# Kernel tuning notes

Measured on AMD Instinct MI355X. Metric: run time of the kernel, lower is better.

Reference implementation:

```python
import jax, jax.numpy as jnp
import numpy as np

NEG_SLOPE = 0.2  # PyG GATConv default leaky_relu slope
EPS = 1e-16     # PyG softmax denominator epsilon


def gat_conv(x, src, dst, W, att_src, att_dst, bias, concat, num_nodes):
    """PyG-style GATConv (eval mode, dropout disabled).
    x: [N, F_in]; W: [F_in, H*C]; att_src/att_dst: [H, C]; bias: [H*C] or [C].
    Messages flow src -> dst; softmax is per destination node."""
    H, C = att_src.shape
    h = (x @ W).reshape(num_nodes, H, C)                      # [N,H,C]
    a_src = jnp.sum(h * att_src[None], axis=-1)               # [N,H]
    a_dst = jnp.sum(h * att_dst[None], axis=-1)               # [N,H]
    e = jax.nn.leaky_relu(a_src[src] + a_dst[dst], NEG_SLOPE) # [E,H]
    # numerically-stable segment softmax over edges grouped by dst
    m = jax.ops.segment_max(e, dst, num_segments=num_nodes)   # [N,H]
    ex = jnp.exp(e - m[dst])                                  # [E,H]
    s = jax.ops.segment_sum(ex, dst, num_segments=num_nodes)  # [N,H]
    alpha = ex / (s[dst] + EPS)                               # [E,H]
    msg = h[src] * alpha[..., None]                           # [E,H,C]
    out = jax.ops.segment_sum(msg, dst, num_segments=num_nodes)  # [N,H,C]
    if concat:
        out = out.reshape(num_nodes, H * C)
    else:
        out = out.mean(axis=1)                                # [N,C]
    return out + bias, alpha


def setup_inputs() -> dict:
    key = jax.random.key(0)
    ks = jax.random.split(key, 20)
    N, E = 50000, 500000
    F_node = 128       # num_node_features
    SED = 128          # sentence_embedding_dim
    HID = 64           # hidden_channels
    H = 2              # num_heads

    def g(k, shape, scale=0.05):
        return jax.random.normal(k, shape, dtype=jnp.float32) * scale

    return {
        "x": jax.random.normal(ks[0], (N, SED), dtype=jnp.float32),
        "edge_index": jax.random.randint(ks[1], (2, E), 0, N, dtype=jnp.int64),
        "cls_emb": jax.random.normal(ks[2], (768,), dtype=jnp.float32),
        # fc0: Linear(768, SED)
        "fc0_w": g(ks[3], (SED, 768)), "fc0_b": g(ks[4], (SED,)),
        # conv1: GATConv(2*SED -> HID, heads=H, concat=True)
        "W1": g(ks[5], (2 * SED, H * HID)),
        "att_src1": g(ks[6], (H, HID)), "att_dst1": g(ks[7], (H, HID)),
        "bias1": g(ks[8], (H * HID,)),
        # conv2: GATConv(H*HID -> F_node, heads=H, concat=False)
        "W2": g(ks[9], (H * HID, H * F_node)),
        "att_src2": g(ks[10], (H, F_node)), "att_dst2": g(ks[11], (H, F_node)),
        "bias2": g(ks[12], (F_node,)),
        # edge MLP head
        "fc2_w": g(ks[13], (F_node, 2 * F_node)), "fc2_b": g(ks[14], (F_node,)),
        "fc3_w": g(ks[15], (1, F_node)), "fc3_b": g(ks[16], (1,)),
    }


def reference(x, edge_index, cls_emb, fc0_w, fc0_b,
              W1, att_src1, att_dst1, bias1,
              W2, att_src2, att_dst2, bias2,
              fc2_w, fc2_b, fc3_w, fc3_b):
    N = x.shape[0]
    src, dst = edge_index[0], edge_index[1]
    # sentence embedding projection + broadcast-concat to every node
    sent = fc0_w @ cls_emb + fc0_b                                # [SED]
    h = jnp.concatenate([x, jnp.broadcast_to(sent, (N, sent.shape[0]))], axis=1)
    h, _ = gat_conv(h, src, dst, W1, att_src1, att_dst1, bias1, True, N)
    h = jax.nn.elu(h)
    h, _ = gat_conv(h, src, dst, W2, att_src2, att_dst2, bias2, False, N)
    # edge head: gather endpoints, concat, MLP, sigmoid
    edge_input = jnp.concatenate([h[src], h[dst]], axis=1)        # [E, 2*F]
    z = jax.nn.relu(edge_input @ fc2_w.T + fc2_b)                 # [E, F]
    logits = z @ fc3_w.T + fc3_b                                  # [E, 1]
    return jax.nn.sigmoid(logits)
```

## Files before the change

### kernel.cpp

```cpp
#include <hip/hip_runtime.h>
#include <hip/hip_bf16.h>
#include <math.h>


typedef short short8 __attribute__((ext_vector_type(8)));
typedef float floatx4 __attribute__((ext_vector_type(4)));

__device__ __forceinline__ float wave_allreduce_sum(float v) {
    #pragma unroll
    for (int off = 1; off < 64; off <<= 1) v += __shfl_xor(v, off, 64);
    return v;
}
__device__ __forceinline__ float bf16lo(unsigned u) {
    unsigned x = u << 16; return __builtin_bit_cast(float, x);
}
__device__ __forceinline__ float bf16hi(unsigned u) {
    unsigned x = u & 0xFFFF0000u; return __builtin_bit_cast(float, x);
}
__device__ __forceinline__ unsigned short bfbits(float f) {
    return __builtin_bit_cast(unsigned short, __float2bfloat16(f));
}
__device__ __forceinline__ unsigned packbf(float a, float b) {
    return ((unsigned)bfbits(b) << 16) | (unsigned)bfbits(a);
}
__device__ __forceinline__ float lrelu(float v) { return v > 0.f ? v : 0.2f * v; }

__global__ void prep_kernel(const float* __restrict__ cls, const float* __restrict__ fc0_w,
                            const float* __restrict__ fc0_b, const float* __restrict__ W1,
                            const float* __restrict__ W2, const float* __restrict__ fc2_w,
                            float* __restrict__ c1,
                            __hip_bfloat16* __restrict__ w1frag,
                            __hip_bfloat16* __restrict__ w2frag,
                            __hip_bfloat16* __restrict__ fc2frag) {
    int tid = threadIdx.x;
    if (blockIdx.x == 0) {
        __shared__ float s_sent[128];
        if (tid < 128) {
            float acc = fc0_b[tid];
            const float* row = fc0_w + (size_t)tid * 768;
            for (int k = 0; k < 768; ++k) acc += row[k] * cls[k];
            s_sent[tid] = acc;
        }
        __syncthreads();
        if (tid < 128) {
            float acc = 0.f;
            for (int k = 0; k < 128; ++k) acc += s_sent[k] * W1[(128 + k) * 128 + tid];
            c1[tid] = acc;
        }
    }
    int gstride = gridDim.x * blockDim.x;
    int g = blockIdx.x * blockDim.x + tid;
    for (int i = g; i < 16384; i += gstride) {
        int j = i & 7, l = (i >> 3) & 63, nt = (i >> 9) & 7, kt = (i >> 12) & 3;
        int k = kt * 32 + (l >> 4) * 8 + j;
        int n = nt * 16 + (l & 15);
        w1frag[i] = __float2bfloat16(W1[k * 128 + n]);
    }
    for (int i = g; i < 32768; i += gstride) {
        int j = i & 7, l = (i >> 3) & 63, nt = (i >> 9) & 15, kt = (i >> 13) & 3;
        int k = kt * 32 + (l >> 4) * 8 + j;
        int n = nt * 16 + (l & 15);
        w2frag[i] = __float2bfloat16(W2[k * 256 + n]);
    }
    for (int i = g; i < 32768; i += gstride) {
        int j = i & 7, l = (i >> 3) & 63, nt = (i >> 9) & 15, kt = (i >> 13) & 3;
        int k = kt * 32 + (l >> 4) * 8 + j;
        int n = nt * 16 + (l & 15);
        float v = (n < 128) ? fc2_w[n * 256 + k] : fc2_w[(n - 128) * 256 + 128 + k];
        fc2frag[i] = __float2bfloat16(v);
    }
}

__global__ void count_kernel(const int* __restrict__ dst, int* __restrict__ counts, int E) {
    int e = blockIdx.x * blockDim.x + threadIdx.x;
    if (e < E) atomicAdd(&counts[dst[e]], 1);
}

__global__ void __launch_bounds__(256) bsum_kernel(const int* __restrict__ counts,
                                                   int* __restrict__ bsum, int N) {
    int base = blockIdx.x * 1024;
    int tid = threadIdx.x;
    int v = 0;
    #pragma unroll
    for (int k = 0; k < 4; ++k) {
        int idx = base + k * 256 + tid;
        if (idx < N) v += counts[idx];
    }
    #pragma unroll
    for (int off = 1; off < 64; off <<= 1) v += __shfl_xor(v, off, 64);
    __shared__ int ws[4];
    if ((tid & 63) == 0) ws[tid >> 6] = v;
    __syncthreads();
    if (tid == 0) bsum[blockIdx.x] = ws[0] + ws[1] + ws[2] + ws[3];
}

__global__ void top_scan_kernel(const int* __restrict__ bsum, int* __restrict__ boff, int nb) {
    int lane = threadIdx.x;
    int v = (lane < nb) ? bsum[lane] : 0;
    int x = v;
    #pragma unroll
    for (int off = 1; off < 64; off <<= 1) {
        int t = __shfl_up(x, off, 64);
        if (lane >= off) x += t;
    }
    if (lane < nb) boff[lane] = x - v;
}

__global__ void __launch_bounds__(1024) local_scan_kernel(const int* __restrict__ counts,
                                                          const int* __restrict__ boff,
                                                          int* __restrict__ row, int* __restrict__ woff,
                                                          int N, int E) {
    int tid = threadIdx.x, lane = tid & 63, wv = tid >> 6;
    int base = blockIdx.x * 1024;
    __shared__ int wsum[16];
    int v = (base + tid < N) ? counts[base + tid] : 0;
    int x = v;
    #pragma unroll
    for (int off = 1; off < 64; off <<= 1) {
        int t = __shfl_up(x, off, 64);
        if (lane >= off) x += t;
    }
    if (lane == 63) wsum[wv] = x;
    __syncthreads();
    if (wv == 0 && lane < 16) {
        int y = wsum[lane];
        #pragma unroll
        for (int off = 1; off < 16; off <<= 1) {
            int t = __shfl_up(y, off, 64);
            if (lane >= off) y += t;
        }
        wsum[lane] = y;
    }
    __syncthreads();
    int excl = boff[blockIdx.x] + (wv ? wsum[wv - 1] : 0) + x - v;
    if (base + tid < N) { row[base + tid] = excl; woff[base + tid] = excl; }
    if (blockIdx.x == 0 && tid == 0) row[N] = E;
}

__global__ void scatter_logit1_kernel(const int* __restrict__ src, const int* __restrict__ dst,
                                      int* __restrict__ woff,
                                      const float* __restrict__ a_s1, const float* __restrict__ a_d1,
                                      int* __restrict__ srcs, float2* __restrict__ ex1,
                                      int* __restrict__ epos, int E) {
    int e = blockIdx.x * blockDim.x + threadIdx.x;
    if (e >= E) return;
    int s = src[e], d = dst[e];
    int pos = atomicAdd(&woff[d], 1);
    epos[e] = pos;
    srcs[pos] = s;
    float2 as = ((const float2*)a_s1)[s];
    float2 ad = ((const float2*)a_d1)[d];
    float2 ex;
    ex.x = __expf(lrelu(as.x + ad.x));
    ex.y = __expf(lrelu(as.y + ad.y));
    ex1[pos] = ex;
}

__global__ void logit2_kernel(const int* __restrict__ src, const int* __restrict__ dst,
                              const int* __restrict__ epos,
                              const float* __restrict__ a_s2, const float* __restrict__ a_d2,
                              float2* __restrict__ ex2, int E) {
    int e = blockIdx.x * blockDim.x + threadIdx.x;
    if (e >= E) return;
    int s = src[e], d = dst[e];
    float2 as = ((const float2*)a_s2)[s];
    float2 ad = ((const float2*)a_d2)[d];
    float2 ex;
    ex.x = __expf(lrelu(as.x + ad.x));
    ex.y = __expf(lrelu(as.y + ad.y));
    ex2[epos[e]] = ex;
}

__global__ void __launch_bounds__(256) gemm1_mfma_kernel(
        const float* __restrict__ x, const __hip_bfloat16* __restrict__ wfrag,
        const float* __restrict__ c1, const float* __restrict__ att_s, const float* __restrict__ att_d,
        __hip_bfloat16* __restrict__ h1bf, float* __restrict__ a_src, float* __restrict__ a_dst, int N) {
    int lane = threadIdx.x & 63, wv = threadIdx.x >> 6;
    int lo = lane & 15, quad = lane >> 4;
    int rowbase = (blockIdx.x * 4 + wv) * 16;
    if (rowbase >= N) return;
    int arow = rowbase + lo; if (arow >= N) arow = N - 1;
    const float* ap = x + (size_t)arow * 128 + quad * 8;
    floatx4 acc[8];
    #pragma unroll
    for (int nt = 0; nt < 8; ++nt) acc[nt] = (floatx4){0.f, 0.f, 0.f, 0.f};
    const short8* bf = (const short8*)wfrag;
    #pragma unroll
    for (int kt = 0; kt < 4; ++kt) {
        float4 fa = *(const float4*)(ap + kt * 32);
        float4 fb = *(const float4*)(ap + kt * 32 + 4);
        short8 a;
        a[0] = (short)bfbits(fa.x); a[1] = (short)bfbits(fa.y);
        a[2] = (short)bfbits(fa.z); a[3] = (short)bfbits(fa.w);
        a[4] = (short)bfbits(fb.x); a[5] = (short)bfbits(fb.y);
        a[6] = (short)bfbits(fb.z); a[7] = (short)bfbits(fb.w);
        #pragma unroll
        for (int nt = 0; nt < 8; ++nt)
            acc[nt] = __builtin_amdgcn_mfma_f32_16x16x32_bf16(a, bf[(kt * 8 + nt) * 64 + lane], acc[nt], 0, 0, 0);
    }
    float ps0[4] = {0,0,0,0}, ps1[4] = {0,0,0,0}, pd0[4] = {0,0,0,0}, pd1[4] = {0,0,0,0};
    #pragma unroll
    for (int nt = 0; nt < 8; ++nt) {
        int ch = nt * 16 + lo;
        float cv = c1[ch], as_v = att_s[ch], ad_v = att_d[ch];
        #pragma unroll
        for (int r = 0; r < 4; ++r) {
            int row = rowbase + quad * 4 + r;
            float val = acc[nt][r] + cv;
            if (row < N) ((unsigned short*)h1bf)[(size_t)row * 128 + ch] = bfbits(val);
            if (nt < 4) { ps0[r] += val * as_v; pd0[r] += val * ad_v; }
            else        { ps1[r] += val * as_v; pd1[r] += val * ad_v; }
        }
    }
    #pragma unroll
    for (int r = 0; r < 4; ++r) {
        int row = rowbase + quad * 4 + r;
        float v0 = ps0[r], v1 = ps1[r], v2 = pd0[r], v3 = pd1[r];
        #pragma unroll
        for (int off = 1; off < 16; off <<= 1) {
            v0 += __shfl_xor(v0, off, 64); v1 += __shfl_xor(v1, off, 64);
            v2 += __shfl_xor(v2, off, 64); v3 += __shfl_xor(v3, off, 64);
        }
        if (lo == 0 && row < N) {
            a_src[row * 2 + 0] = v0; a_src[row * 2 + 1] = v1;
            a_dst[row * 2 + 0] = v2; a_dst[row * 2 + 1] = v3;
        }
    }
}

__global__ void __launch_bounds__(256) agg1_csr_kernel(
        const int* __restrict__ row, const int* __restrict__ srcs, const float2* __restrict__ ex1,
        const unsigned* __restrict__ h1u, const float* __restrict__ bias1,
        unsigned* __restrict__ hmid_u, int N) {
    int d = blockIdx.x * 4 + (threadIdx.x >> 6);
    if (d >= N) return;
    int lane = threadIdx.x & 63;
    int beg = row[d], end = row[d + 1];
    int g = lane >> 4, q = lane & 15;
    float den0 = 0.f, den1 = 0.f;
    float facc[8];
    #pragma unroll
    for (int m = 0; m < 8; ++m) facc[m] = 0.f;
    for (int b = beg; b < end; b += 64) {
        int i = b + lane;
        int s = 0; float e0 = 0.f, e1 = 0.f;
        if (i < end) {
            s = srcs[i];
            float2 ex = ex1[i];
            e0 = ex.x; e1 = ex.y;
            den0 += e0; den1 += e1;
        }
        int cnt = min(64, end - b);
        int rounds = (cnt + 3) >> 2;
        for (int j = 0; j < rounds; ++j) {
            int sl = 4 * j + g;
            float w0 = __shfl(e0, sl, 64);
            float w1 = __shfl(e1, sl, 64);
            int   sj = __shfl(s,  sl, 64);
            float wgt = (q < 8) ? w0 : w1;
            uint4 u = ((const uint4*)(h1u + (size_t)sj * 64))[q];
            facc[0] += bf16lo(u.x) * wgt; facc[1] += bf16hi(u.x) * wgt;
            facc[2] += bf16lo(u.y) * wgt; facc[3] += bf16hi(u.y) * wgt;
            facc[4] += bf16lo(u.z) * wgt; facc[5] += bf16hi(u.z) * wgt;
            facc[6] += bf16lo(u.w) * wgt; facc[7] += bf16hi(u.w) * wgt;
        }
    }
    den0 = wave_allreduce_sum(den0);
    den1 = wave_allreduce_sum(den1);
    #pragma unroll
    for (int m = 0; m < 8; ++m) {
        facc[m] += __shfl_xor(facc[m], 16, 64);
        facc[m] += __shfl_xor(facc[m], 32, 64);
    }
    if (lane < 16) {
        float inv = (lane < 8) ? 1.f / (den0 + 1e-16f) : 1.f / (den1 + 1e-16f);
        int c0 = 8 * lane;
        float v[8];
        #pragma unroll
        for (int m = 0; m < 8; ++m) {
            float vv = facc[m] * inv + bias1[c0 + m];
            v[m] = vv > 0.f ? vv : expm1f(vv);
        }
        uint4 o;
        o.x = packbf(v[0], v[1]); o.y = packbf(v[2], v[3]);
        o.z = packbf(v[4], v[5]); o.w = packbf(v[6], v[7]);
        ((uint4*)(hmid_u + (size_t)d * 64))[lane] = o;
    }
}

__global__ void __launch_bounds__(256) gemm2_mfma_kernel(
        const __hip_bfloat16* __restrict__ hmid, const __hip_bfloat16* __restrict__ wfrag,
        const float* __restrict__ att_s, const float* __restrict__ att_d,
        __hip_bfloat16* __restrict__ h2pre, float* __restrict__ a_src, float* __restrict__ a_dst, int N) {
    int lane = threadIdx.x & 63, wv = threadIdx.x >> 6;
    int lo = lane & 15, quad = lane >> 4;
    int rowbase = (blockIdx.x * 4 + wv) * 16;
    if (rowbase >= N) return;
    int arow = rowbase + lo; if (arow >= N) arow = N - 1;
    const __hip_bfloat16* ap = hmid + (size_t)arow * 128 + quad * 8;
    floatx4 acc[16];
    #pragma unroll
    for (int nt = 0; nt < 16; ++nt) acc[nt] = (floatx4){0.f, 0.f, 0.f, 0.f};
    const short8* bf = (const short8*)wfrag;
    #pragma unroll
    for (int kt = 0; kt < 4; ++kt) {
        short8 a = *(const short8*)(ap + kt * 32);
        #pragma unroll
        for (int nt = 0; nt < 16; ++nt)
            acc[nt] = __builtin_amdgcn_mfma_f32_16x16x32_bf16(a, bf[(kt * 16 + nt) * 64 + lane], acc[nt], 0, 0, 0);
    }
    float ps0[4] = {0,0,0,0}, ps1[4] = {0,0,0,0}, pd0[4] = {0,0,0,0}, pd1[4] = {0,0,0,0};
    #pragma unroll
    for (int nt = 0; nt < 16; ++nt) {
        int ch = nt * 16 + lo;
        float as_v = att_s[ch], ad_v = att_d[ch];
        #pragma unroll
        for (int r = 0; r < 4; ++r) {
            int row = rowbase + quad * 4 + r;
            float val = acc[nt][r];
            if (row < N) ((unsigned short*)h2pre)[(size_t)row * 256 + ch] = bfbits(val);
            if (nt < 8) { ps0[r] += val * as_v; pd0[r] += val * ad_v; }
            else        { ps1[r] += val * as_v; pd1[r] += val * ad_v; }
        }
    }
    #pragma unroll
    for (int r = 0; r < 4; ++r) {
        int row = rowbase + quad * 4 + r;
        float v0 = ps0[r], v1 = ps1[r], v2 = pd0[r], v3 = pd1[r];
        #pragma unroll
        for (int off = 1; off < 16; off <<= 1) {
            v0 += __shfl_xor(v0, off, 64); v1 += __shfl_xor(v1, off, 64);
            v2 += __shfl_xor(v2, off, 64); v3 += __shfl_xor(v3, off, 64);
        }
        if (lo == 0 && row < N) {
            a_src[row * 2 + 0] = v0; a_src[row * 2 + 1] = v1;
            a_dst[row * 2 + 0] = v2; a_dst[row * 2 + 1] = v3;
        }
    }
}

__global__ void __launch_bounds__(256) agg2_csr_kernel(
        const int* __restrict__ row, const int* __restrict__ srcs, const float2* __restrict__ ex2,
        const unsigned* __restrict__ h2u, const float* __restrict__ bias2,
        unsigned* __restrict__ h2bf_u, int N) {
    int d = blockIdx.x * 4 + (threadIdx.x >> 6);
    if (d >= N) return;
    int lane = threadIdx.x & 63;
    int beg = row[d], end = row[d + 1];
    int g = lane >> 5, q = lane & 31;
    float den0 = 0.f, den1 = 0.f;
    float facc[8];
    #pragma unroll
    for (int m = 0; m < 8; ++m) facc[m] = 0.f;
    for (int b = beg; b < end; b += 64) {
        int i = b + lane;
        int s = 0; float e0 = 0.f, e1 = 0.f;
        if (i < end) {
            s = srcs[i];
            float2 ex = ex2[i];
            e0 = ex.x; e1 = ex.y;
            den0 += e0; den1 += e1;
        }
        int cnt = min(64, end - b);
        int rounds = (cnt + 1) >> 1;
        for (int j = 0; j < rounds; ++j) {
            int sl = 2 * j + g;
            float w0 = __shfl(e0, sl, 64);
            float w1 = __shfl(e1, sl, 64);
            int   sj = __shfl(s,  sl, 64);
            float wgt = (q < 16) ? w0 : w1;
            uint4 u = ((const uint4*)(h2u + (size_t)sj * 128))[q];
            facc[0] += bf16lo(u.x) * wgt; facc[1] += bf16hi(u.x) * wgt;
            facc[2] += bf16lo(u.y) * wgt; facc[3] += bf16hi(u.y) * wgt;
            facc[4] += bf16lo(u.z) * wgt; facc[5] += bf16hi(u.z) * wgt;
            facc[6] += bf16lo(u.w) * wgt; facc[7] += bf16hi(u.w) * wgt;
        }
    }
    den0 = wave_allreduce_sum(den0);
    den1 = wave_allreduce_sum(den1);
    float inv = (q < 16) ? 0.5f / (den0 + 1e-16f) : 0.5f / (den1 + 1e-16f);
    #pragma unroll
    for (int m = 0; m < 8; ++m) {
        facc[m] += __shfl_xor(facc[m], 32, 64);
        facc[m] *= inv;
        facc[m] += __shfl_xor(facc[m], 16, 64);
    }
    if (lane < 16) {
        int c0 = 8 * lane;
        uint4 o;
        o.x = packbf(facc[0] + bias2[c0 + 0], facc[1] + bias2[c0 + 1]);
        o.y = packbf(facc[2] + bias2[c0 + 2], facc[3] + bias2[c0 + 3]);
        o.z = packbf(facc[4] + bias2[c0 + 4], facc[5] + bias2[c0 + 5]);
        o.w = packbf(facc[6] + bias2[c0 + 6], facc[7] + bias2[c0 + 7]);
        ((uint4*)(h2bf_u + (size_t)d * 64))[lane] = o;
    }
}

__global__ void __launch_bounds__(256) zsd_mfma_kernel(
        const __hip_bfloat16* __restrict__ h2bf, const __hip_bfloat16* __restrict__ wfrag,
        const float* __restrict__ fc2_b, __hip_bfloat16* __restrict__ zsd, int N) {
    int lane = threadIdx.x & 63, wv = threadIdx.x >> 6;
    int lo = lane & 15, quad = lane >> 4;
    int rowbase = (blockIdx.x * 4 + wv) * 16;
    if (rowbase >= N) return;
    int arow = rowbase + lo; if (arow >= N) arow = N - 1;
    const __hip_bfloat16* ap = h2bf + (size_t)arow * 128 + quad * 8;
    floatx4 acc[16];
    #pragma unroll
    for (int nt = 0; nt < 16; ++nt) acc[nt] = (floatx4){0.f, 0.f, 0.f, 0.f};
    const short8* bf = (const short8*)wfrag;
    #pragma unroll
    for (int kt = 0; kt < 4; ++kt) {
        short8 a = *(const short8*)(ap + kt * 32);
        #pragma unroll
        for (int nt = 0; nt < 16; ++nt)
            acc[nt] = __builtin_amdgcn_mfma_f32_16x16x32_bf16(a, bf[(kt * 16 + nt) * 64 + lane], acc[nt], 0, 0, 0);
    }
    #pragma unroll
    for (int nt = 0; nt < 16; ++nt) {
        int ch = nt * 16 + lo;
        float bv = (nt >= 8) ? fc2_b[ch - 128] : 0.f;
        #pragma unroll
        for (int r = 0; r < 4; ++r) {
            int row = rowbase + quad * 4 + r;
            if (row < N) ((unsigned short*)zsd)[(size_t)row * 256 + ch] = bfbits(acc[nt][r] + bv);
        }
    }
}

__global__ void __launch_bounds__(256) edge_zsd_kernel(
        const int* __restrict__ src, const int* __restrict__ dst,
        const unsigned* __restrict__ zsd_u, const float* __restrict__ fc3_w,
        const float* __restrict__ fc3_b, float* __restrict__ out, int E) {
    int lane = threadIdx.x & 63, wv = threadIdx.x >> 6;
    int g = lane >> 5, r = (lane >> 4) & 1, q = lane & 15;
    int base = (blockIdx.x * 4 + wv) * 16;
    if (base >= E) return;
    float f3[8];
    #pragma unroll
    for (int m = 0; m < 8; ++m) f3[m] = fc3_w[8 * q + m];
    float b3 = fc3_b[0];
    #pragma unroll
    for (int j = 0; j < 8; ++j) {
        int e = base + 2 * j + g;
        int ec = e < E ? e : E - 1;
        int node = r ? dst[ec] : src[ec];
        uint4 mine = ((const uint4*)(zsd_u + (size_t)node * 128 + (r << 6)))[q];
        uint4 oth;
        oth.x = (unsigned)__shfl_xor((int)mine.x, 16, 64);
        oth.y = (unsigned)__shfl_xor((int)mine.y, 16, 64);
        oth.z = (unsigned)__shfl_xor((int)mine.z, 16, 64);
        oth.w = (unsigned)__shfl_xor((int)mine.w, 16, 64);
        float p = 0.f;
        p += fmaxf(bf16lo(mine.x) + bf16lo(oth.x), 0.f) * f3[0];
        p += fmaxf(bf16hi(mine.x) + bf16hi(oth.x), 0.f) * f3[1];
        p += fmaxf(bf16lo(mine.y) + bf16lo(oth.y), 0.f) * f3[2];
        p += fmaxf(bf16hi(mine.y) + bf16hi(oth.y), 0.f) * f3[3];
        p += fmaxf(bf16lo(mine.z) + bf16lo(oth.z), 0.f) * f3[4];
        p += fmaxf(bf16hi(mine.z) + bf16hi(oth.z), 0.f) * f3[5];
        p += fmaxf(bf16lo(mine.w) + bf16lo(oth.w), 0.f) * f3[6];
        p += fmaxf(bf16hi(mine.w) + bf16hi(oth.w), 0.f) * f3[7];
        #pragma unroll
        for (int off = 1; off < 32; off <<= 1) p += __shfl_xor(p, off, 64);
        if ((lane & 31) == 0 && e < E)
            out[e] = 1.f / (1.f + expf(-(0.5f * p + b3)));
    }
}

extern "C" void kernel_launch(void* const* d_in, const int* in_sizes, int n_in,
                              void* d_out, int out_size, void* d_ws, size_t ws_size,
                              hipStream_t stream) {
    const float* x      = (const float*)d_in[0];
    const int*   ei     = (const int*)d_in[1];
    const float* cls    = (const float*)d_in[2];
    const float* fc0_w  = (const float*)d_in[3];
    const float* fc0_b  = (const float*)d_in[4];
    const float* W1     = (const float*)d_in[5];
    const float* att_s1 = (const float*)d_in[6];
    const float* att_d1 = (const float*)d_in[7];
    const float* bias1  = (const float*)d_in[8];
    const float* W2     = (const float*)d_in[9];
    const float* att_s2 = (const float*)d_in[10];
    const float* att_d2 = (const float*)d_in[11];
    const float* bias2  = (const float*)d_in[12];
    const float* fc2_w  = (const float*)d_in[13];
    const float* fc2_b  = (const float*)d_in[14];
    const float* fc3_w  = (const float*)d_in[15];
    const float* fc3_b  = (const float*)d_in[16];
    float* out = (float*)d_out;

    int N = in_sizes[0] / 128;
    int E = in_sizes[1] / 2;
    const int* src = ei;
    const int* dst = ei + E;
    int nb = (N + 1023) / 1024;

    float* w = (float*)d_ws;
    size_t off = 0;
    auto alloc = [&](size_t n) { float* p = w + off; off += (n + 63) & ~(size_t)63; return p; };
    float* c1      = alloc(128);
    float* w1fragf = alloc(16384 / 2);
    float* w2fragf = alloc(32768 / 2);
    float* fc2fragf= alloc(32768 / 2);
    float* a_s1    = alloc((size_t)N * 2);
    float* a_d1    = alloc((size_t)N * 2);
    float* a_s2    = alloc((size_t)N * 2);
    float* a_d2    = alloc((size_t)N * 2);
    float* h1bff   = alloc((size_t)N * 64);
    float* hmidf   = alloc((size_t)N * 64);
    float* h2pref  = alloc((size_t)N * 128);
    float* h2bff   = alloc((size_t)N * 64);
    float* zsdf    = alloc((size_t)N * 128);
    float* ex1f    = alloc((size_t)E * 2);
    float* ex2f    = alloc((size_t)E * 2);
    int* counts = (int*)alloc(N);
    int* rowp   = (int*)alloc(N + 1);
    int* woff   = (int*)alloc(N);
    int* srcs   = (int*)alloc(E);
    int* epos   = (int*)alloc(E);
    int* bsum   = (int*)alloc(64);
    int* boff   = (int*)alloc(64);
    __hip_bfloat16* w1frag = (__hip_bfloat16*)w1fragf;
    __hip_bfloat16* w2frag = (__hip_bfloat16*)w2fragf;
    __hip_bfloat16* fc2frag= (__hip_bfloat16*)fc2fragf;
    __hip_bfloat16* h1bf   = (__hip_bfloat16*)h1bff;
    __hip_bfloat16* hmid   = (__hip_bfloat16*)hmidf;
    __hip_bfloat16* h2pre  = (__hip_bfloat16*)h2pref;
    __hip_bfloat16* h2bf   = (__hip_bfloat16*)h2bff;
    __hip_bfloat16* zsd    = (__hip_bfloat16*)zsdf;

    hipMemsetAsync(counts, 0, sizeof(int) * (size_t)N, stream);

    prep_kernel<<<64, 256, 0, stream>>>(cls, fc0_w, fc0_b, W1, W2, fc2_w, c1, w1frag, w2frag, fc2frag);
    count_kernel<<<(E + 255) / 256, 256, 0, stream>>>(dst, counts, E);
    bsum_kernel<<<nb, 256, 0, stream>>>(counts, bsum, N);
    top_scan_kernel<<<1, 64, 0, stream>>>(bsum, boff, nb);
    local_scan_kernel<<<nb, 1024, 0, stream>>>(counts, boff, rowp, woff, N, E);
    gemm1_mfma_kernel<<<(N + 63) / 64, 256, 0, stream>>>(x, w1frag, c1, att_s1, att_d1, h1bf, a_s1, a_d1, N);
    scatter_logit1_kernel<<<(E + 255) / 256, 256, 0, stream>>>(src, dst, woff, a_s1, a_d1, srcs, (float2*)ex1f, epos, E);
    agg1_csr_kernel<<<(N + 3) / 4, 256, 0, stream>>>(rowp, srcs, (const float2*)ex1f, (const unsigned*)h1bf, bias1, (unsigned*)hmid, N);
    gemm2_mfma_kernel<<<(N + 63) / 64, 256, 0, stream>>>(hmid, w2frag, att_s2, att_d2, h2pre, a_s2, a_d2, N);
    logit2_kernel<<<(E + 255) / 256, 256, 0, stream>>>(src, dst, epos, a_s2, a_d2, (float2*)ex2f, E);
    agg2_csr_kernel<<<(N + 3) / 4, 256, 0, stream>>>(rowp, srcs, (const float2*)ex2f, (const unsigned*)h2pre, bias2, (unsigned*)h2bf, N);
    zsd_mfma_kernel<<<(N + 63) / 64, 256, 0, stream>>>(h2bf, fc2frag, fc2_b, zsd, N);
    edge_zsd_kernel<<<(E + 63) / 64, 256, 0, stream>>>(src, dst, (const unsigned*)zsd, fc3_w, fc3_b, out, E);
}
```

Baseline: 375.5 us.

## Fuse edge logits into CSR aggregation, single-block scan, prefetch gathers, packed math

Drops the separate per-edge logit kernels and their ex/epos buffers, and computes the exp-logits inside the aggregation kernels from a_src/a_dst. The three-kernel scan becomes a single 1024-thread block that loops over all nodes. Scatter now only writes srcs. The aggregation inner loops software-prefetch the next neighbour row and accumulate with packed float2 math, and the edge head splits its fc3 work across the two half-waves. The single-block scan serialises about 50 iterations, which risks a longer latency for that step than the old multi-block scan.

```diff
diff --git a/kernel.cpp b/kernel.cpp
--- a/kernel.cpp
+++ b/kernel.cpp
@@ -5,6 +5,8 @@
 
 typedef short short8 __attribute__((ext_vector_type(8)));
 typedef float floatx4 __attribute__((ext_vector_type(4)));
+typedef float v2f __attribute__((ext_vector_type(2)));
+typedef unsigned uint2v __attribute__((ext_vector_type(2)));
 
 __device__ __forceinline__ float wave_allreduce_sum(float v) {
     #pragma unroll
@@ -16,6 +18,10 @@
 }
 __device__ __forceinline__ float bf16hi(unsigned u) {
     unsigned x = u & 0xFFFF0000u; return __builtin_bit_cast(float, x);
+}
+__device__ __forceinline__ v2f bfpair(unsigned v) {
+    uint2v t; t.x = v << 16; t.y = v & 0xFFFF0000u;
+    return __builtin_bit_cast(v2f, t);
 }
 __device__ __forceinline__ unsigned short bfbits(float f) {
     return __builtin_bit_cast(unsigned short, __float2bfloat16(f));
@@ -76,99 +82,51 @@
     if (e < E) atomicAdd(&counts[dst[e]], 1);
 }
 
-__global__ void __launch_bounds__(256) bsum_kernel(const int* __restrict__ counts,
-                                                   int* __restrict__ bsum, int N) {
-    int base = blockIdx.x * 1024;
-    int tid = threadIdx.x;
-    int v = 0;
-    #pragma unroll
-    for (int k = 0; k < 4; ++k) {
-        int idx = base + k * 256 + tid;
-        if (idx < N) v += counts[idx];
-    }
-    #pragma unroll
-    for (int off = 1; off < 64; off <<= 1) v += __shfl_xor(v, off, 64);
-    __shared__ int ws[4];
-    if ((tid & 63) == 0) ws[tid >> 6] = v;
+__global__ void __launch_bounds__(1024) scan_kernel(const int* __restrict__ counts,
+                                                    int* __restrict__ row, int* __restrict__ woff,
+                                                    int N, int E) {
+    int tid = threadIdx.x, lane = tid & 63, wv = tid >> 6;
+    __shared__ int wsum[16];
+    __shared__ int carry;
+    if (tid == 0) carry = 0;
     __syncthreads();
-    if (tid == 0) bsum[blockIdx.x] = ws[0] + ws[1] + ws[2] + ws[3];
-}
-
-__global__ void top_scan_kernel(const int* __restrict__ bsum, int* __restrict__ boff, int nb) {
-    int lane = threadIdx.x;
-    int v = (lane < nb) ? bsum[lane] : 0;
-    int x = v;
-    #pragma unroll
-    for (int off = 1; off < 64; off <<= 1) {
-        int t = __shfl_up(x, off, 64);
-        if (lane >= off) x += t;
-    }
-    if (lane < nb) boff[lane] = x - v;
-}
-
-__global__ void __launch_bounds__(1024) local_scan_kernel(const int* __restrict__ counts,
-                                                          const int* __restrict__ boff,
-                                                          int* __restrict__ row, int* __restrict__ woff,
-                                                          int N, int E) {
-    int tid = threadIdx.x, lane = tid & 63, wv = tid >> 6;
-    int base = blockIdx.x * 1024;
-    __shared__ int wsum[16];
-    int v = (base + tid < N) ? counts[base + tid] : 0;
-    int x = v;
-    #pragma unroll
-    for (int off = 1; off < 64; off <<= 1) {
-        int t = __shfl_up(x, off, 64);
-        if (lane >= off) x += t;
-    }
-    if (lane == 63) wsum[wv] = x;
-    __syncthreads();
-    if (wv == 0 && lane < 16) {
-        int y = wsum[lane];
-        #pragma unroll
-        for (int off = 1; off < 16; off <<= 1) {
-            int t = __shfl_up(y, off, 64);
-            if (lane >= off) y += t;
-        }
-        wsum[lane] = y;
-    }
-    __syncthreads();
-    int excl = boff[blockIdx.x] + (wv ? wsum[wv - 1] : 0) + x - v;
-    if (base + tid < N) { row[base + tid] = excl; woff[base + tid] = excl; }
-    if (blockIdx.x == 0 && tid == 0) row[N] = E;
-}
-
-__global__ void scatter_logit1_kernel(const int* __restrict__ src, const int* __restrict__ dst,
-                                      int* __restrict__ woff,
-                                      const float* __restrict__ a_s1, const float* __restrict__ a_d1,
-                                      int* __restrict__ srcs, float2* __restrict__ ex1,
-                                      int* __restrict__ epos, int E) {
+    for (int base = 0; base < N; base += 1024) {
+        int v = (base + tid < N) ? counts[base + tid] : 0;
+        int x = v;
+        #pragma unroll
+        for (int off = 1; off < 64; off <<= 1) {
+            int t = __shfl_up(x, off, 64);
+            if (lane >= off) x += t;
+        }
+        if (lane == 63) wsum[wv] = x;
+        __syncthreads();
+        if (wv == 0 && lane < 16) {
+            int y = wsum[lane];
+            #pragma unroll
+            for (int off = 1; off < 16; off <<= 1) {
+                int t = __shfl_up(y, off, 64);
+                if (lane >= off) y += t;
+            }
+            wsum[lane] = y;
+        }
+        __syncthreads();
+        int wexcl = (wv == 0) ? 0 : wsum[wv - 1];
+        int excl = carry + wexcl + x - v;
+        if (base + tid < N) { row[base + tid] = excl; woff[base + tid] = excl; }
+        __syncthreads();
+        if (tid == 0) carry += wsum[15];
+        __syncthreads();
+    }
+    if (tid == 0) row[N] = E;
+}
+
+__global__ void scatter_kernel(const int* __restrict__ src, const int* __restrict__ dst,
+                               int* __restrict__ woff, int* __restrict__ srcs, int E) {
     int e = blockIdx.x * blockDim.x + threadIdx.x;
-    if (e >= E) return;
-    int s = src[e], d = dst[e];
-    int pos = atomicAdd(&woff[d], 1);
-    epos[e] = pos;
-    srcs[pos] = s;
-    float2 as = ((const float2*)a_s1)[s];
-    float2 ad = ((const float2*)a_d1)[d];
-    float2 ex;
-    ex.x = __expf(lrelu(as.x + ad.x));
-    ex.y = __expf(lrelu(as.y + ad.y));
-    ex1[pos] = ex;
-}
-
-__global__ void logit2_kernel(const int* __restrict__ src, const int* __restrict__ dst,
-                              const int* __restrict__ epos,
-                              const float* __restrict__ a_s2, const float* __restrict__ a_d2,
-                              float2* __restrict__ ex2, int E) {
-    int e = blockIdx.x * blockDim.x + threadIdx.x;
-    if (e >= E) return;
-    int s = src[e], d = dst[e];
-    float2 as = ((const float2*)a_s2)[s];
-    float2 ad = ((const float2*)a_d2)[d];
-    float2 ex;
-    ex.x = __expf(lrelu(as.x + ad.x));
-    ex.y = __expf(lrelu(as.y + ad.y));
-    ex2[epos[e]] = ex;
+    if (e < E) {
+        int pos = atomicAdd(&woff[dst[e]], 1);
+        srcs[pos] = src[e];
+    }
 }
 
 __global__ void __launch_bounds__(256) gemm1_mfma_kernel(
@@ -229,7 +187,8 @@
 }
 
 __global__ void __launch_bounds__(256) agg1_csr_kernel(
-        const int* __restrict__ row, const int* __restrict__ srcs, const float2* __restrict__ ex1,
+        const int* __restrict__ row, const int* __restrict__ srcs,
+        const float* __restrict__ a_src, const float* __restrict__ a_dst,
         const unsigned* __restrict__ h1u, const float* __restrict__ bias1,
         unsigned* __restrict__ hmid_u, int N) {
     int d = blockIdx.x * 4 + (threadIdx.x >> 6);
@@ -237,49 +196,61 @@
     int lane = threadIdx.x & 63;
     int beg = row[d], end = row[d + 1];
     int g = lane >> 4, q = lane & 15;
+    float2 adp = ((const float2*)a_dst)[d];
     float den0 = 0.f, den1 = 0.f;
-    float facc[8];
-    #pragma unroll
-    for (int m = 0; m < 8; ++m) facc[m] = 0.f;
+    v2f facc2[4];
+    #pragma unroll
+    for (int m = 0; m < 4; ++m) facc2[m] = (v2f){0.f, 0.f};
     for (int b = beg; b < end; b += 64) {
         int i = b + lane;
         int s = 0; float e0 = 0.f, e1 = 0.f;
         if (i < end) {
             s = srcs[i];
-            float2 ex = ex1[i];
-            e0 = ex.x; e1 = ex.y;
+            float2 as = ((const float2*)a_src)[s];
+            e0 = __expf(lrelu(as.x + adp.x));
+            e1 = __expf(lrelu(as.y + adp.y));
             den0 += e0; den1 += e1;
         }
         int cnt = min(64, end - b);
         int rounds = (cnt + 3) >> 2;
+        float w0 = __shfl(e0, g, 64);
+        float w1 = __shfl(e1, g, 64);
+        int   sj = __shfl(s,  g, 64);
+        float wgt = (q < 8) ? w0 : w1;
+        uint4 u = ((const uint4*)(h1u + (size_t)sj * 64))[q];
         for (int j = 0; j < rounds; ++j) {
-            int sl = 4 * j + g;
-            float w0 = __shfl(e0, sl, 64);
-            float w1 = __shfl(e1, sl, 64);
-            int   sj = __shfl(s,  sl, 64);
-            float wgt = (q < 8) ? w0 : w1;
-            uint4 u = ((const uint4*)(h1u + (size_t)sj * 64))[q];
-            facc[0] += bf16lo(u.x) * wgt; facc[1] += bf16hi(u.x) * wgt;
-            facc[2] += bf16lo(u.y) * wgt; facc[3] += bf16hi(u.y) * wgt;
-            facc[4] += bf16lo(u.z) * wgt; facc[5] += bf16hi(u.z) * wgt;
-            facc[6] += bf16lo(u.w) * wgt; facc[7] += bf16hi(u.w) * wgt;
+            int sl2 = 4 * j + 4 + g; sl2 = sl2 > 63 ? 63 : sl2;
+            float w0n = __shfl(e0, sl2, 64);
+            float w1n = __shfl(e1, sl2, 64);
+            int   sjn = __shfl(s,  sl2, 64);
+            uint4 un = ((const uint4*)(h1u + (size_t)sjn * 64))[q];
+            float wgtn = (q < 8) ? w0n : w1n;
+            facc2[0] += bfpair(u.x) * wgt;
+            facc2[1] += bfpair(u.y) * wgt;
+            facc2[2] += bfpair(u.z) * wgt;
+            facc2[3] += bfpair(u.w) * wgt;
+            u = un; wgt = wgtn;
         }
     }
     den0 = wave_allreduce_sum(den0);
     den1 = wave_allreduce_sum(den1);
     #pragma unroll
-    for (int m = 0; m < 8; ++m) {
-        facc[m] += __shfl_xor(facc[m], 16, 64);
-        facc[m] += __shfl_xor(facc[m], 32, 64);
+    for (int m = 0; m < 4; ++m) {
+        facc2[m].x += __shfl_xor(facc2[m].x, 16, 64);
+        facc2[m].y += __shfl_xor(facc2[m].y, 16, 64);
+        facc2[m].x += __shfl_xor(facc2[m].x, 32, 64);
+        facc2[m].y += __shfl_xor(facc2[m].y, 32, 64);
     }
     if (lane < 16) {
         float inv = (lane < 8) ? 1.f / (den0 + 1e-16f) : 1.f / (den1 + 1e-16f);
         int c0 = 8 * lane;
         float v[8];
         #pragma unroll
-        for (int m = 0; m < 8; ++m) {
-            float vv = facc[m] * inv + bias1[c0 + m];
-            v[m] = vv > 0.f ? vv : expm1f(vv);
+        for (int m = 0; m < 4; ++m) {
+            float va = facc2[m].x * inv + bias1[c0 + 2 * m];
+            float vb = facc2[m].y * inv + bias1[c0 + 2 * m + 1];
+            v[2 * m]     = va > 0.f ? va : expm1f(va);
+            v[2 * m + 1] = vb > 0.f ? vb : expm1f(vb);
         }
         uint4 o;
         o.x = packbf(v[0], v[1]); o.y = packbf(v[2], v[3]);
@@ -340,7 +311,8 @@
 }
 
 __global__ void __launch_bounds__(256) agg2_csr_kernel(
-        const int* __restrict__ row, const int* __restrict__ srcs, const float2* __restrict__ ex2,
+        const int* __restrict__ row, const int* __restrict__ srcs,
+        const float* __restrict__ a_src, const float* __restrict__ a_dst,
         const unsigned* __restrict__ h2u, const float* __restrict__ bias2,
         unsigned* __restrict__ h2bf_u, int N) {
     int d = blockIdx.x * 4 + (threadIdx.x >> 6);
@@ -348,50 +320,60 @@
     int lane = threadIdx.x & 63;
     int beg = row[d], end = row[d + 1];
     int g = lane >> 5, q = lane & 31;
+    float2 adp = ((const float2*)a_dst)[d];
     float den0 = 0.f, den1 = 0.f;
-    float facc[8];
-    #pragma unroll
-    for (int m = 0; m < 8; ++m) facc[m] = 0.f;
+    v2f facc2[4];
+    #pragma unroll
+    for (int m = 0; m < 4; ++m) facc2[m] = (v2f){0.f, 0.f};
     for (int b = beg; b < end; b += 64) {
         int i = b + lane;
         int s = 0; float e0 = 0.f, e1 = 0.f;
         if (i < end) {
             s = srcs[i];
-            float2 ex = ex2[i];
-            e0 = ex.x; e1 = ex.y;
+            float2 as = ((const float2*)a_src)[s];
+            e0 = __expf(lrelu(as.x + adp.x));
+            e1 = __expf(lrelu(as.y + adp.y));
             den0 += e0; den1 += e1;
         }
         int cnt = min(64, end - b);
         int rounds = (cnt + 1) >> 1;
+        float w0 = __shfl(e0, g, 64);
+        float w1 = __shfl(e1, g, 64);
+        int   sj = __shfl(s,  g, 64);
+        float wgt = (q < 16) ? w0 : w1;
+        uint4 u = ((const uint4*)(h2u + (size_t)sj * 128))[q];
         for (int j = 0; j < rounds; ++j) {
-            int sl = 2 * j + g;
-            float w0 = __shfl(e0, sl, 64);
-            float w1 = __shfl(e1, sl, 64);
-            int   sj = __shfl(s,  sl, 64);
-            float wgt = (q < 16) ? w0 : w1;
-            uint4 u = ((const uint4*)(h2u + (size_t)sj * 128))[q];
-            facc[0] += bf16lo(u.x) * wgt; facc[1] += bf16hi(u.x) * wgt;
-            facc[2] += bf16lo(u.y) * wgt; facc[3] += bf16hi(u.y) * wgt;
-            facc[4] += bf16lo(u.z) * wgt; facc[5] += bf16hi(u.z) * wgt;
-            facc[6] += bf16lo(u.w) * wgt; facc[7] += bf16hi(u.w) * wgt;
+            int sl2 = 2 * j + 2 + g; sl2 = sl2 > 63 ? 63 : sl2;
+            float w0n = __shfl(e0, sl2, 64);
+            float w1n = __shfl(e1, sl2, 64);
+            int   sjn = __shfl(s,  sl2, 64);
+            uint4 un = ((const uint4*)(h2u + (size_t)sjn * 128))[q];
+            float wgtn = (q < 16) ? w0n : w1n;
+            facc2[0] += bfpair(u.x) * wgt;
+            facc2[1] += bfpair(u.y) * wgt;
+            facc2[2] += bfpair(u.z) * wgt;
+            facc2[3] += bfpair(u.w) * wgt;
+            u = un; wgt = wgtn;
         }
     }
     den0 = wave_allreduce_sum(den0);
     den1 = wave_allreduce_sum(den1);
     float inv = (q < 16) ? 0.5f / (den0 + 1e-16f) : 0.5f / (den1 + 1e-16f);
     #pragma unroll
-    for (int m = 0; m < 8; ++m) {
-        facc[m] += __shfl_xor(facc[m], 32, 64);
-        facc[m] *= inv;
-        facc[m] += __shfl_xor(facc[m], 16, 64);
+    for (int m = 0; m < 4; ++m) {
+        facc2[m].x += __shfl_xor(facc2[m].x, 32, 64);
+        facc2[m].y += __shfl_xor(facc2[m].y, 32, 64);
+        facc2[m] *= inv;
+        facc2[m].x += __shfl_xor(facc2[m].x, 16, 64);
+        facc2[m].y += __shfl_xor(facc2[m].y, 16, 64);
     }
     if (lane < 16) {
         int c0 = 8 * lane;
         uint4 o;
-        o.x = packbf(facc[0] + bias2[c0 + 0], facc[1] + bias2[c0 + 1]);
-        o.y = packbf(facc[2] + bias2[c0 + 2], facc[3] + bias2[c0 + 3]);
-        o.z = packbf(facc[4] + bias2[c0 + 4], facc[5] + bias2[c0 + 5]);
-        o.w = packbf(facc[6] + bias2[c0 + 6], facc[7] + bias2[c0 + 7]);
+        o.x = packbf(facc2[0].x + bias2[c0 + 0], facc2[0].y + bias2[c0 + 1]);
+        o.y = packbf(facc2[1].x + bias2[c0 + 2], facc2[1].y + bias2[c0 + 3]);
+        o.z = packbf(facc2[2].x + bias2[c0 + 4], facc2[2].y + bias2[c0 + 5]);
+        o.w = packbf(facc2[3].x + bias2[c0 + 6], facc2[3].y + bias2[c0 + 7]);
         ((uint4*)(h2bf_u + (size_t)d * 64))[lane] = o;
     }
 }
@@ -436,9 +418,8 @@
     int g = lane >> 5, r = (lane >> 4) & 1, q = lane & 15;
     int base = (blockIdx.x * 4 + wv) * 16;
     if (base >= E) return;
-    float f3[8];
-    #pragma unroll
-    for (int m = 0; m < 8; ++m) f3[m] = fc3_w[8 * q + m];
+    v2f f30 = {fc3_w[8 * q + 4 * r + 0], fc3_w[8 * q + 4 * r + 1]};
+    v2f f31 = {fc3_w[8 * q + 4 * r + 2], fc3_w[8 * q + 4 * r + 3]};
     float b3 = fc3_b[0];
     #pragma unroll
     for (int j = 0; j < 8; ++j) {
@@ -446,24 +427,24 @@
         int ec = e < E ? e : E - 1;
         int node = r ? dst[ec] : src[ec];
         uint4 mine = ((const uint4*)(zsd_u + (size_t)node * 128 + (r << 6)))[q];
-        uint4 oth;
-        oth.x = (unsigned)__shfl_xor((int)mine.x, 16, 64);
-        oth.y = (unsigned)__shfl_xor((int)mine.y, 16, 64);
-        oth.z = (unsigned)__shfl_xor((int)mine.z, 16, 64);
-        oth.w = (unsigned)__shfl_xor((int)mine.w, 16, 64);
-        float p = 0.f;
-        p += fmaxf(bf16lo(mine.x) + bf16lo(oth.x), 0.f) * f3[0];
-        p += fmaxf(bf16hi(mine.x) + bf16hi(oth.x), 0.f) * f3[1];
-        p += fmaxf(bf16lo(mine.y) + bf16lo(oth.y), 0.f) * f3[2];
-        p += fmaxf(bf16hi(mine.y) + bf16hi(oth.y), 0.f) * f3[3];
-        p += fmaxf(bf16lo(mine.z) + bf16lo(oth.z), 0.f) * f3[4];
-        p += fmaxf(bf16hi(mine.z) + bf16hi(oth.z), 0.f) * f3[5];
-        p += fmaxf(bf16lo(mine.w) + bf16lo(oth.w), 0.f) * f3[6];
-        p += fmaxf(bf16hi(mine.w) + bf16hi(oth.w), 0.f) * f3[7];
+        unsigned sx = (unsigned)__shfl_xor((int)mine.x, 16, 64);
+        unsigned sy = (unsigned)__shfl_xor((int)mine.y, 16, 64);
+        unsigned sz = (unsigned)__shfl_xor((int)mine.z, 16, 64);
+        unsigned sw = (unsigned)__shfl_xor((int)mine.w, 16, 64);
+        unsigned mA = r ? mine.z : mine.x;
+        unsigned mB = r ? mine.w : mine.y;
+        unsigned oA = r ? sz : sx;
+        unsigned oB = r ? sw : sy;
+        v2f sA = bfpair(mA) + bfpair(oA);
+        v2f sB = bfpair(mB) + bfpair(oB);
+        sA.x = fmaxf(sA.x, 0.f); sA.y = fmaxf(sA.y, 0.f);
+        sB.x = fmaxf(sB.x, 0.f); sB.y = fmaxf(sB.y, 0.f);
+        v2f p2 = sA * f30 + sB * f31;
+        float p = p2.x + p2.y;
         #pragma unroll
         for (int off = 1; off < 32; off <<= 1) p += __shfl_xor(p, off, 64);
         if ((lane & 31) == 0 && e < E)
-            out[e] = 1.f / (1.f + expf(-(0.5f * p + b3)));
+            out[e] = 1.f / (1.f + expf(-(p + b3)));
     }
 }
 
@@ -493,7 +474,6 @@
     int E = in_sizes[1] / 2;
     const int* src = ei;
     const int* dst = ei + E;
-    int nb = (N + 1023) / 1024;
 
     float* w = (float*)d_ws;
     size_t off = 0;
@@ -511,37 +491,29 @@
     float* h2pref  = alloc((size_t)N * 128);
     float* h2bff   = alloc((size_t)N * 64);
     float* zsdf    = alloc((size_t)N * 128);
-    float* ex1f    = alloc((size_t)E * 2);
-    float* ex2f    = alloc((size_t)E * 2);
     int* counts = (int*)alloc(N);
     int* rowp   = (int*)alloc(N + 1);
     int* woff   = (int*)alloc(N);
     int* srcs   = (int*)alloc(E);
-    int* epos   = (int*)alloc(E);
-    int* bsum   = (int*)alloc(64);
-    int* boff   = (int*)alloc(64);
     __hip_bfloat16* w1frag = (__hip_bfloat16*)w1fragf;
     __hip_bfloat16* w2frag = (__hip_bfloat16*)w2fragf;
     __hip_bfloat16* fc2frag= (__hip_bfloat16*)fc2fragf;
-    __hip_bfloat16* h1bf   = (__hip_bfloat16*)h1bff;
     __hip_bfloat16* hmid   = (__hip_bfloat16*)hmidf;
     __hip_bfloat16* h2pre  = (__hip_bfloat16*)h2pref;
     __hip_bfloat16* h2bf   = (__hip_bfloat16*)h2bff;
+    __hip_bfloat16* h1bf   = (__hip_bfloat16*)h1bff;
     __hip_bfloat16* zsd    = (__hip_bfloat16*)zsdf;
 
     hipMemsetAsync(counts, 0, sizeof(int) * (size_t)N, stream);
 
     prep_kernel<<<64, 256, 0, stream>>>(cls, fc0_w, fc0_b, W1, W2, fc2_w, c1, w1frag, w2frag, fc2frag);
     count_kernel<<<(E + 255) / 256, 256, 0, stream>>>(dst, counts, E);
-    bsum_kernel<<<nb, 256, 0, stream>>>(counts, bsum, N);
-    top_scan_kernel<<<1, 64, 0, stream>>>(bsum, boff, nb);
-    local_scan_kernel<<<nb, 1024, 0, stream>>>(counts, boff, rowp, woff, N, E);
+    scan_kernel<<<1, 1024, 0, stream>>>(counts, rowp, woff, N, E);
+    scatter_kernel<<<(E + 255) / 256, 256, 0, stream>>>(src, dst, woff, srcs, E);
     gemm1_mfma_kernel<<<(N + 63) / 64, 256, 0, stream>>>(x, w1frag, c1, att_s1, att_d1, h1bf, a_s1, a_d1, N);
-    scatter_logit1_kernel<<<(E + 255) / 256, 256, 0, stream>>>(src, dst, woff, a_s1, a_d1, srcs, (float2*)ex1f, epos, E);
-    agg1_csr_kernel<<<(N + 3) / 4, 256, 0, stream>>>(rowp, srcs, (const float2*)ex1f, (const unsigned*)h1bf, bias1, (unsigned*)hmid, N);
+    agg1_csr_kernel<<<(N + 3) / 4, 256, 0, stream>>>(rowp, srcs, a_s1, a_d1, (const unsigned*)h1bf, bias1, (unsigned*)hmid, N);
     gemm2_mfma_kernel<<<(N + 63) / 64, 256, 0, stream>>>(hmid, w2frag, att_s2, att_d2, h2pre, a_s2, a_d2, N);
-    logit2_kernel<<<(E + 255) / 256, 256, 0, stream>>>(src, dst, epos, a_s2, a_d2, (float2*)ex2f, E);
-    agg2_csr_kernel<<<(N + 3) / 4, 256, 0, stream>>>(rowp, srcs, (const float2*)ex2f, (const unsigned*)h2pre, bias2, (unsigned*)h2bf, N);
+    agg2_csr_kernel<<<(N + 3) / 4, 256, 0, stream>>>(rowp, srcs, a_s2, a_d2, (const unsigned*)h2pre, bias2, (unsigned*)h2bf, N);
     zsd_mfma_kernel<<<(N + 63) / 64, 256, 0, stream>>>(h2bf, fc2frag, fc2_b, zsd, N);
     edge_zsd_kernel<<<(E + 63) / 64, 256, 0, stream>>>(src, dst, (const unsigned*)zsd, fc3_w, fc3_b, out, E);
 }
```

After: 406.5 us. 8.2% more time.
